# Optimization experiments

Hardware: AMD Instinct MI355X
Metric: run time of the kernel (lower is better)

## Reference

```python
import jax, jax.numpy as jnp
import numpy as np

B_SZ, NP, NTOK, D, H, DH, D2 = 8192, 10, 21, 128, 2, 64, 32
EPS = 1e-8
PATCH_POS = np.array([2 * k - 1 for k in range(1, NP + 1)])  # [1,3,...,19]
STAT_POS = np.array([0] + [2 * k for k in range(1, NP + 1)])  # [0,2,...,20]


def setup_inputs() -> dict:
    key = jax.random.key(0)
    ks = jax.random.split(key, 12)
    x = jax.random.normal(ks[0], (B_SZ, NTOK, D), jnp.float32)
    # rotary frequencies: unit-magnitude complex exp(i * pos * theta)
    inv_freq = 1.0 / (10000.0 ** (jnp.arange(D2, dtype=jnp.float32) / D2))
    ang = jnp.arange(NTOK, dtype=jnp.float32)[:, None] * inv_freq[None, :]  # [N, d2]
    fc_real, fc_imag = jnp.cos(ang), jnp.sin(ang)
    s = 1.0 / np.sqrt(D)
    g = 1.0 + 0.02 * jax.random.normal(ks[1], (D,), jnp.float32)
    Wqkv = s * jax.random.normal(ks[2], (D, 3 * D), jnp.float32)
    bqkv = jnp.zeros((3 * D,), jnp.float32)
    Wout = s * jax.random.normal(ks[3], (D, D), jnp.float32)
    bout = jnp.zeros((D,), jnp.float32)
    Wg = s * jax.random.normal(ks[4], (D, D), jnp.float32)
    bg = jnp.zeros((D,), jnp.float32)
    Wr = s * jax.random.normal(ks[5], (D, D), jnp.float32)
    br = jnp.zeros((D,), jnp.float32)
    # learned bias B: decoupled init 0.0, coupled patch<->stat pairs 2.0
    Bb = np.zeros((NTOK, NTOK), np.float32)
    Bb[PATCH_POS, STAT_POS[1:]] = 2.0
    Bb[STAT_POS[1:], PATCH_POS] = 2.0
    return dict(x=x, fc_real=fc_real, fc_imag=fc_imag, g=g, Wqkv=Wqkv, bqkv=bqkv,
                Wout=Wout, bout=bout, Wg=Wg, bg=bg, Wr=Wr, br=br, Bbias=jnp.asarray(Bb))


def _zcrmsnorm(x, g):
    x0 = x - x.mean(-1, keepdims=True)
    return x0 / jnp.sqrt(jnp.mean(x0 * x0, -1, keepdims=True) + EPS) * g


def _rope(t, fr, fi):
    # t: [B,H,N,DH] viewed as complex pairs [B,H,N,d2,2]; fr/fi: [N,d2]
    tr = t.reshape(*t.shape[:-1], D2, 2)
    a, b = tr[..., 0], tr[..., 1]
    out = jnp.stack([a * fr - b * fi, a * fi + b * fr], axis=-1)
    return out.reshape(t.shape)


def reference(x, fc_real, fc_imag, g, Wqkv, bqkv, Wout, bout, Wg, bg, Wr, br, Bbias):
    B, N, Dm = x.shape
    h = _zcrmsnorm(x, g)
    qkv = (h @ Wqkv + bqkv).reshape(B, N, 3, H, DH)
    q = qkv[:, :, 0].transpose(0, 2, 1, 3)  # [B,H,N,DH]
    k = qkv[:, :, 1].transpose(0, 2, 1, 3)
    v = qkv[:, :, 2].transpose(0, 2, 1, 3)
    fr, fi = fc_real[:N], fc_imag[:N]
    q, k = _rope(q, fr, fi), _rope(k, fr, fi)
    scale = 1.0 / np.sqrt(DH)
    scores = jnp.einsum('bhnd,bhmd->bhnm', q, k) * scale + Bbias[None, None]
    a_full = jax.nn.softmax(scores, axis=-1)
    y_full = jnp.einsum('bhnm,bhmd->bhnd', a_full, v)
    y_full = y_full.transpose(0, 2, 1, 3).reshape(B, N, Dm) @ Wout + bout
    # patch -> stat attention
    q_p, k_s, v_s = q[:, :, PATCH_POS], k[:, :, STAT_POS], v[:, :, STAT_POS]
    sc2 = jnp.einsum('bhnd,bhmd->bhnm', q_p, k_s) * scale
    a2 = jax.nn.softmax(sc2, axis=-1)
    y2 = jnp.einsum('bhnm,bhmd->bhnd', a2, v_s).transpose(0, 2, 1, 3).reshape(B, NP, Dm)
    y2 = y2 @ Wr + br
    h_patch = h[:, PATCH_POS]  # [B,NP,D]
    norms = jnp.linalg.norm(h_patch, axis=-1, keepdims=True)
    uncertainty = 1.0 - jax.nn.sigmoid(norms - norms.mean())
    gate = jax.nn.sigmoid(h_patch @ Wg + bg) * uncertainty
    y = y_full.at[:, PATCH_POS, :].add(gate * y2)
    return x + y
```

## Files before the change

### kernel.cpp

```cpp
#include <hip/hip_runtime.h>
#include <math.h>

#define NB   8192
#define NTOK 21
#define NP   10

typedef __bf16 bf16_t;
typedef __bf16 bf16x8 __attribute__((ext_vector_type(8)));
typedef __bf16 bf16x4 __attribute__((ext_vector_type(4)));
typedef float  f32x4  __attribute__((ext_vector_type(4)));

#define ROW128(r,c) ((r)*128 + ((c) ^ (((r)&7)<<3)))
#define VTIDX(d,m)  ((d)*32  + ((m) ^ (((d)&3)<<3)))
#define ATIDX(r,m)  ((r)*32  + ((m) ^ (((r)&3)<<3)))

#define MFMA(a,b,c) __builtin_amdgcn_mfma_f32_16x16x32_bf16((a),(b),(c),0,0,0)

__global__ __launch_bounds__(256) void k_wconv(
    const float* __restrict__ Wqkv, const float* __restrict__ Wout,
    const float* __restrict__ Wg,   const float* __restrict__ Wr,
    bf16_t* __restrict__ wq, bf16_t* __restrict__ wo,
    bf16_t* __restrict__ wgb, bf16_t* __restrict__ wrb)
{
    int i = blockIdx.x * 256 + threadIdx.x;
    if (i < 49152) {
        int k = i / 384, n = i - k * 384;
        wq[((k >> 3) * 384 + n) * 8 + (k & 7)] = (bf16_t)Wqkv[i];
    } else {
        int j = i - 49152;
        int sel = j >> 14;
        int t = j & 16383;
        int k = t >> 7, n = t & 127;
        const float* src = sel == 0 ? Wout : (sel == 1 ? Wg : Wr);
        bf16_t* dst = sel == 0 ? wo : (sel == 1 ? wgb : wrb);
        dst[((k >> 3) * 128 + n) * 8 + (k & 7)] = (bf16_t)src[t];
    }
}

__global__ __launch_bounds__(256) void k_norms(const float* __restrict__ x,
                                               const float* __restrict__ g,
                                               float* __restrict__ part)
{
    __shared__ float sd[4];
    const int wave = threadIdx.x >> 6, lane = threadIdx.x & 63;
    const int row = blockIdx.x * 4 + wave;
    const int b = row / NP, p = row - b * NP;
    const float* xr = x + (size_t)b * 2688 + (2 * p + 1) * 128;
    float a0 = xr[lane], a1 = xr[lane + 64];
    float s = a0 + a1, sq = a0 * a0 + a1 * a1;
    #pragma unroll
    for (int off = 32; off; off >>= 1) { s += __shfl_xor(s, off); sq += __shfl_xor(sq, off); }
    float mean = s * (1.0f / 128);
    float rstd = rsqrtf(sq * (1.0f / 128) - mean * mean + 1e-8f);
    float h0 = (a0 - mean) * rstd * g[lane];
    float h1 = (a1 - mean) * rstd * g[lane + 64];
    float n2 = h0 * h0 + h1 * h1;
    #pragma unroll
    for (int off = 32; off; off >>= 1) n2 += __shfl_xor(n2, off);
    if (lane == 0) sd[wave] = sqrtf(n2);
    __syncthreads();
    if (threadIdx.x == 0)
        atomicAdd(&part[(blockIdx.x & 63) * 16], sd[0] + sd[1] + sd[2] + sd[3]);
}

__global__ __launch_bounds__(256, 4) void k_main(
    const float* __restrict__ x,   const float* __restrict__ fcr,
    const float* __restrict__ fci, const float* __restrict__ g,
    const float* __restrict__ bqkv, const float* __restrict__ bout,
    const float* __restrict__ bg,   const float* __restrict__ br,
    const float* __restrict__ Bb,   const float* __restrict__ part,
    const bf16_t* __restrict__ wq,  const bf16_t* __restrict__ wo,
    const bf16_t* __restrict__ wgb, const bf16_t* __restrict__ wrb,
    float* __restrict__ out)
{
    __shared__ __align__(16) bf16_t hsb[32 * 128];
    __shared__ __align__(16) bf16_t reg1[32 * 128];
    __shared__ __align__(16) bf16_t reg2[32 * 128];
    __shared__ __align__(16) bf16_t reg3[128 * 32];
    __shared__ __align__(16) char  pool[5376];
    __shared__ float normv[11];

    float* fcs  = (float*)pool;
    float* fis  = (float*)pool + 672;
    float* att  = (float*)pool;
    float* att2 = (float*)(pool + 3696);
    bf16_t* y2bb = (bf16_t*)pool;

    const int tid = threadIdx.x;
    const int w = tid >> 6, l = tid & 63, l15 = l & 15, gq = l >> 4;
    const int b = blockIdx.x;
    const float* xb = x + (size_t)b * 2688;

    {
        const float4* c4 = (const float4*)fcr; float4* dc = (float4*)fcs;
        const float4* i4 = (const float4*)fci; float4* di = (float4*)fis;
        if (tid < 168) { dc[tid] = c4[tid]; di[tid] = i4[tid]; }
        for (int i = tid; i < 11 * 128; i += 256)
            hsb[(21 + (i >> 7)) * 128 + (i & 127)] = (bf16_t)0.f;
        if (tid < 64) {
            float s = part[tid * 16];
            #pragma unroll
            for (int off = 32; off; off >>= 1) s += __shfl_xor(s, off);
            if (tid == 0) normv[10] = s * (1.f / 81920.f);
        }
        for (int r = w; r < 21; r += 4) {
            float a0 = xb[r * 128 + l], a1 = xb[r * 128 + 64 + l];
            float s = a0 + a1, sq = a0 * a0 + a1 * a1;
            #pragma unroll
            for (int off = 32; off; off >>= 1) { s += __shfl_xor(s, off); sq += __shfl_xor(sq, off); }
            float mean = s * (1.0f / 128);
            float rstd = rsqrtf(sq * (1.0f / 128) - mean * mean + 1e-8f);
            float h0 = (a0 - mean) * rstd * g[l];
            float h1 = (a1 - mean) * rstd * g[l + 64];
            hsb[ROW128(r, l)]      = (bf16_t)h0;
            hsb[ROW128(r, l + 64)] = (bf16_t)h1;
            if (r & 1) {
                float n2 = h0 * h0 + h1 * h1;
                #pragma unroll
                for (int off = 32; off; off >>= 1) n2 += __shfl_xor(n2, off);
                if (l == 0) normv[r >> 1] = sqrtf(n2);
            }
        }
    }
    __syncthreads();

    {
        bf16x8 afr[2][4];
        #pragma unroll
        for (int mt = 0; mt < 2; mt++)
            #pragma unroll
            for (int ks = 0; ks < 4; ks++)
                afr[mt][ks] = *(const bf16x8*)&hsb[ROW128(mt * 16 + l15, ks * 32 + gq * 8)];
        #pragma unroll 2
        for (int q6 = 0; q6 < 6; ++q6) {
            int nt = w * 6 + q6;
            int n = nt * 16 + l15;
            bf16x8 bfr[4];
            #pragma unroll
            for (int ks = 0; ks < 4; ks++)
                bfr[ks] = *(const bf16x8*)&wq[((ks * 4 + gq) * 384 + n) * 8];
            float bias = bqkv[n];
            #pragma unroll
            for (int mt = 0; mt < 2; mt++) {
                f32x4 acc = {0.f, 0.f, 0.f, 0.f};
                #pragma unroll
                for (int ks = 0; ks < 4; ks++) acc = MFMA(afr[mt][ks], bfr[ks], acc);
                int rbase = mt * 16 + gq * 4;
                if (n < 256) {
                    int d = n & 63, j = d >> 1;
                    bool ev = !(d & 1);
                    bf16_t* dst = (n < 128) ? reg1 : reg2;
                    int cc = n & 127;
                    #pragma unroll
                    for (int i = 0; i < 4; i++) {
                        int r = rbase + i; int rr = r < 21 ? r : 0;
                        float v = acc[i] + bias;
                        float p = __shfl_xor(v, 1);
                        float fr = fcs[rr * 32 + j], fi = fis[rr * 32 + j];
                        float o = ev ? (v * fr - p * fi) : (p * fi + v * fr);
                        dst[ROW128(r, cc)] = (bf16_t)o;
                    }
                } else {
                    int d = n - 256;
                    bf16x4 pv;
                    #pragma unroll
                    for (int i = 0; i < 4; i++) pv[i] = (bf16_t)(acc[i] + bias);
                    *(bf16x4*)&reg3[VTIDX(d, rbase)] = pv;
                }
            }
        }
    }
    __syncthreads();

    {
        #pragma unroll
        for (int q2 = 0; q2 < 2; q2++) {
            int t = w * 2 + q2;
            int hh = t >> 2, mt = (t >> 1) & 1, nt = t & 1;
            f32x4 acc = {0.f, 0.f, 0.f, 0.f};
            #pragma unroll
            for (int ks = 0; ks < 2; ks++) {
                bf16x8 a  = *(const bf16x8*)&reg1[ROW128(mt * 16 + l15, hh * 64 + ks * 32 + gq * 8)];
                bf16x8 bb = *(const bf16x8*)&reg2[ROW128(nt * 16 + l15, hh * 64 + ks * 32 + gq * 8)];
                acc = MFMA(a, bb, acc);
            }
            int m = nt * 16 + l15;
            if (m < 21) {
                #pragma unroll
                for (int i = 0; i < 4; i++) {
                    int n = mt * 16 + gq * 4 + i;
                    if (n < 21) att[hh * 462 + n * 22 + m] = acc[i] * 0.125f + Bb[n * 21 + m];
                }
            }
        }
        if (w < 2) {
            int hh = w;
            int ra = 2 * l15 + 1; if (ra > 20) ra = 20;
            int rb = 2 * l15;     if (rb > 20) rb = 20;
            f32x4 acc = {0.f, 0.f, 0.f, 0.f};
            #pragma unroll
            for (int ks = 0; ks < 2; ks++) {
                bf16x8 a  = *(const bf16x8*)&reg1[ROW128(ra, hh * 64 + ks * 32 + gq * 8)];
                bf16x8 bb = *(const bf16x8*)&reg2[ROW128(rb, hh * 64 + ks * 32 + gq * 8)];
                acc = MFMA(a, bb, acc);
            }
            int s = l15;
            if (s < 11) {
                #pragma unroll
                for (int i = 0; i < 4; i++) {
                    int p = gq * 4 + i;
                    if (p < 10) att2[hh * 120 + p * 12 + s] = acc[i] * 0.125f;
                }
            }
        }
    }
    __syncthreads();

    if (tid < 42) {
        int hh = tid / 21, n = tid - hh * 21;
        float* row = &att[hh * 462 + n * 22];
        float mx = -1e30f;
        for (int m = 0; m < 21; m++) mx = fmaxf(mx, row[m]);
        float s = 0.f;
        for (int m = 0; m < 21; m++) { float e = __expf(row[m] - mx); row[m] = e; s += e; }
        float inv = 1.f / s;
        for (int m = 0; m < 21; m++) row[m] *= inv;
    } else if (tid >= 64 && tid < 84) {
        int t2 = tid - 64, hh = t2 / 10, p = t2 - hh * 10;
        float* row = &att2[hh * 120 + p * 12];
        float mx = -1e30f;
        for (int m = 0; m < 11; m++) mx = fmaxf(mx, row[m]);
        float s = 0.f;
        for (int m = 0; m < 11; m++) { float e = __expf(row[m] - mx); row[m] = e; s += e; }
        float inv = 1.f / s;
        for (int m = 0; m < 11; m++) row[m] *= inv;
    }
    __syncthreads();

    {
        bf16_t* attb  = reg1;
        bf16_t* att2e = reg1 + 2048;
        for (int i = tid; i < 2048; i += 256) {
            int hh = i >> 10, r = (i >> 5) & 31, m = i & 31;
            float v = (r < 21 && m < 21) ? att[hh * 462 + r * 22 + m] : 0.f;
            attb[hh * 1024 + ATIDX(r, m)] = (bf16_t)v;
        }
        for (int i = tid; i < 1024; i += 256) {
            int hh = i >> 9, p = (i >> 5) & 15, m = i & 31;
            float v = (p < 10 && m < 21 && !(m & 1)) ? att2[hh * 120 + p * 12 + (m >> 1)] : 0.f;
            att2e[hh * 512 + ATIDX(p, m)] = (bf16_t)v;
        }
    }
    __syncthreads();

    {
        bf16_t* attb  = reg1;
        bf16_t* att2e = reg1 + 2048;
        for (int t = w * 6; t < w * 6 + 6; ++t) {
            int hh, dloc, mt = 0, isY2;
            if (t < 16) { hh = t >> 3; mt = (t >> 2) & 1; dloc = hh * 64 + (t & 3) * 16 + l15; isY2 = 0; }
            else        { int u = t - 16; hh = u >> 2;    dloc = hh * 64 + (u & 3) * 16 + l15; isY2 = 1; }
            bf16x8 a;
            if (!isY2) { int r = mt * 16 + l15; a = *(const bf16x8*)&attb[hh * 1024 + ATIDX(r, gq * 8)]; }
            else       {                        a = *(const bf16x8*)&att2e[hh * 512 + ATIDX(l15, gq * 8)]; }
            bf16x8 bb = *(const bf16x8*)&reg3[VTIDX(dloc, gq * 8)];
            f32x4 acc = {0.f, 0.f, 0.f, 0.f};
            acc = MFMA(a, bb, acc);
            if (!isY2) {
                #pragma unroll
                for (int i = 0; i < 4; i++) reg2[ROW128(mt * 16 + gq * 4 + i, dloc)] = (bf16_t)acc[i];
            } else {
                #pragma unroll
                for (int i = 0; i < 4; i++) {
                    int rr2 = gq * 4 + i;
                    if (rr2 < 10) y2bb[ROW128(rr2, dloc)] = (bf16_t)acc[i];
                }
            }
        }
    }
    __syncthreads();

    {
        float mn = normv[10];
        float* gyb = (float*)reg3;
        #pragma unroll
        for (int q2 = 0; q2 < 2; q2++) {
            int nt = w * 2 + q2;
            int n = nt * 16 + l15;
            int yrow = l15 < 10 ? l15 : 0;
            f32x4 accg = {0.f, 0.f, 0.f, 0.f}, accr = {0.f, 0.f, 0.f, 0.f};
            #pragma unroll
            for (int ks = 0; ks < 4; ks++) {
                bf16x8 wgf = *(const bf16x8*)&wgb[((ks * 4 + gq) * 128 + n) * 8];
                bf16x8 wrf = *(const bf16x8*)&wrb[((ks * 4 + gq) * 128 + n) * 8];
                bf16x8 ha  = *(const bf16x8*)&hsb[ROW128(2 * l15 + 1, ks * 32 + gq * 8)];
                bf16x8 ya  = *(const bf16x8*)&y2bb[ROW128(yrow, ks * 32 + gq * 8)];
                accg = MFMA(ha, wgf, accg);
                accr = MFMA(ya, wrf, accr);
            }
            float bgc = bg[n], brc = br[n];
            #pragma unroll
            for (int i = 0; i < 4; i++) {
                int p = gq * 4 + i;
                if (p < 10) {
                    float gate = 1.f / (1.f + __expf(-(accg[i] + bgc)));
                    float u = 1.f - 1.f / (1.f + __expf(-(normv[p] - mn)));
                    gyb[p * 128 + n] = u * gate * (accr[i] + brc);
                }
            }
        }
    }
    __syncthreads();

    {
        float* gyb = (float*)reg3;
        float* ob = out + (size_t)b * 2688;
        for (int t = w * 4; t < w * 4 + 4; ++t) {
            int mt = t >> 3, nt = t & 7;
            int n = nt * 16 + l15;
            f32x4 acc = {0.f, 0.f, 0.f, 0.f};
            #pragma unroll
            for (int ks = 0; ks < 4; ks++) {
                bf16x8 a  = *(const bf16x8*)&reg2[ROW128(mt * 16 + l15, ks * 32 + gq * 8)];
                bf16x8 wf = *(const bf16x8*)&wo[((ks * 4 + gq) * 128 + n) * 8];
                acc = MFMA(a, wf, acc);
            }
            float bo = bout[n];
            #pragma unroll
            for (int i = 0; i < 4; i++) {
                int r = mt * 16 + gq * 4 + i;
                if (r < 21) {
                    float v = xb[r * 128 + n] + acc[i] + bo;
                    if (r & 1) v += gyb[((r - 1) >> 1) * 128 + n];
                    ob[r * 128 + n] = v;
                }
            }
        }
    }
}

extern "C" void kernel_launch(void* const* d_in, const int* in_sizes, int n_in,
                              void* d_out, int out_size, void* d_ws, size_t ws_size,
                              hipStream_t stream)
{
    (void)in_sizes; (void)n_in; (void)out_size; (void)ws_size;
    const float* x    = (const float*)d_in[0];
    const float* fcr  = (const float*)d_in[1];
    const float* fci  = (const float*)d_in[2];
    const float* g    = (const float*)d_in[3];
    const float* Wqkv = (const float*)d_in[4];
    const float* bqkv = (const float*)d_in[5];
    const float* Wout = (const float*)d_in[6];
    const float* bout = (const float*)d_in[7];
    const float* Wg   = (const float*)d_in[8];
    const float* bg   = (const float*)d_in[9];
    const float* Wr   = (const float*)d_in[10];
    const float* br   = (const float*)d_in[11];
    const float* Bb   = (const float*)d_in[12];
    float* out = (float*)d_out;

    char* wsb = (char*)d_ws;
    float* part = (float*)wsb;
    bf16_t* wq  = (bf16_t*)(wsb + 4096);
    bf16_t* wo  = wq + 49152;
    bf16_t* wgb = wo + 16384;
    bf16_t* wrb = wgb + 16384;

    hipMemsetAsync(part, 0, 4096, stream);
    hipLaunchKernelGGL(k_wconv, dim3(384),   dim3(256), 0, stream, Wqkv, Wout, Wg, Wr, wq, wo, wgb, wrb);
    hipLaunchKernelGGL(k_norms, dim3(20480), dim3(256), 0, stream, x, g, part);
    hipLaunchKernelGGL(k_main,  dim3(NB),    dim3(256), 0, stream,
                       x, fcr, fci, g, bqkv, bout, bg, br, Bb, part, wq, wo, wgb, wrb, out);
}
```

Before: 376.1 us.

## Fuse softmax into score MFMA epilogue and merge prep kernels

Merges the weight conversion and patch-norm kernels into one launch, with each norm block now handling 32 rows instead of 4. This cuts launch count and the number of atomics. In the main kernel, softmax for both attention paths now runs in registers with 16-lane shuffles right after the score MFMAs and writes bf16 probabilities straight into the swizzled MFMA operand layout. That removes the fp32 score buffer, a serial 42-thread softmax, a conversion pass and two barriers. In exchange it adds shuffles and uses more shared pool memory, which could affect occupancy.

```diff
diff --git a/kernel.cpp b/kernel.cpp
--- a/kernel.cpp
+++ b/kernel.cpp
@@ -16,51 +16,57 @@
 
 #define MFMA(a,b,c) __builtin_amdgcn_mfma_f32_16x16x32_bf16((a),(b),(c),0,0,0)
 
-__global__ __launch_bounds__(256) void k_wconv(
+__global__ __launch_bounds__(256) void k_prep(
     const float* __restrict__ Wqkv, const float* __restrict__ Wout,
     const float* __restrict__ Wg,   const float* __restrict__ Wr,
+    const float* __restrict__ x,    const float* __restrict__ g,
     bf16_t* __restrict__ wq, bf16_t* __restrict__ wo,
-    bf16_t* __restrict__ wgb, bf16_t* __restrict__ wrb)
-{
-    int i = blockIdx.x * 256 + threadIdx.x;
-    if (i < 49152) {
-        int k = i / 384, n = i - k * 384;
-        wq[((k >> 3) * 384 + n) * 8 + (k & 7)] = (bf16_t)Wqkv[i];
-    } else {
-        int j = i - 49152;
-        int sel = j >> 14;
-        int t = j & 16383;
-        int k = t >> 7, n = t & 127;
-        const float* src = sel == 0 ? Wout : (sel == 1 ? Wg : Wr);
-        bf16_t* dst = sel == 0 ? wo : (sel == 1 ? wgb : wrb);
-        dst[((k >> 3) * 128 + n) * 8 + (k & 7)] = (bf16_t)src[t];
-    }
-}
-
-__global__ __launch_bounds__(256) void k_norms(const float* __restrict__ x,
-                                               const float* __restrict__ g,
-                                               float* __restrict__ part)
+    bf16_t* __restrict__ wgb, bf16_t* __restrict__ wrb,
+    float* __restrict__ part)
 {
     __shared__ float sd[4];
-    const int wave = threadIdx.x >> 6, lane = threadIdx.x & 63;
-    const int row = blockIdx.x * 4 + wave;
-    const int b = row / NP, p = row - b * NP;
-    const float* xr = x + (size_t)b * 2688 + (2 * p + 1) * 128;
-    float a0 = xr[lane], a1 = xr[lane + 64];
-    float s = a0 + a1, sq = a0 * a0 + a1 * a1;
-    #pragma unroll
-    for (int off = 32; off; off >>= 1) { s += __shfl_xor(s, off); sq += __shfl_xor(sq, off); }
-    float mean = s * (1.0f / 128);
-    float rstd = rsqrtf(sq * (1.0f / 128) - mean * mean + 1e-8f);
-    float h0 = (a0 - mean) * rstd * g[lane];
-    float h1 = (a1 - mean) * rstd * g[lane + 64];
-    float n2 = h0 * h0 + h1 * h1;
-    #pragma unroll
-    for (int off = 32; off; off >>= 1) n2 += __shfl_xor(n2, off);
-    if (lane == 0) sd[wave] = sqrtf(n2);
-    __syncthreads();
-    if (threadIdx.x == 0)
-        atomicAdd(&part[(blockIdx.x & 63) * 16], sd[0] + sd[1] + sd[2] + sd[3]);
+    if (blockIdx.x < 384) {
+        int i = blockIdx.x * 256 + threadIdx.x;
+        if (i < 49152) {
+            int k = i / 384, n = i - k * 384;
+            wq[((k >> 3) * 384 + n) * 8 + (k & 7)] = (bf16_t)Wqkv[i];
+        } else {
+            int j = i - 49152;
+            int sel = j >> 14;
+            int t = j & 16383;
+            int k = t >> 7, n = t & 127;
+            const float* src = sel == 0 ? Wout : (sel == 1 ? Wg : Wr);
+            bf16_t* dst = sel == 0 ? wo : (sel == 1 ? wgb : wrb);
+            dst[((k >> 3) * 128 + n) * 8 + (k & 7)] = (bf16_t)src[t];
+        }
+    } else {
+        const int nb = blockIdx.x - 384;
+        const int wave = threadIdx.x >> 6, lane = threadIdx.x & 63;
+        const float g0v = g[lane], g1v = g[lane + 64];
+        float acc = 0.f;
+        #pragma unroll
+        for (int rr = 0; rr < 8; rr++) {
+            int row = nb * 32 + wave * 8 + rr;
+            int b = row / NP, p = row - b * NP;
+            const float* xr = x + (size_t)b * 2688 + (2 * p + 1) * 128;
+            float a0 = xr[lane], a1 = xr[lane + 64];
+            float s = a0 + a1, sq = a0 * a0 + a1 * a1;
+            #pragma unroll
+            for (int off = 32; off; off >>= 1) { s += __shfl_xor(s, off); sq += __shfl_xor(sq, off); }
+            float mean = s * (1.0f / 128);
+            float rstd = rsqrtf(sq * (1.0f / 128) - mean * mean + 1e-8f);
+            float h0 = (a0 - mean) * rstd * g0v;
+            float h1 = (a1 - mean) * rstd * g1v;
+            float n2 = h0 * h0 + h1 * h1;
+            #pragma unroll
+            for (int off = 32; off; off >>= 1) n2 += __shfl_xor(n2, off);
+            if (lane == 0) acc += sqrtf(n2);
+        }
+        if (lane == 0) sd[wave] = acc;
+        __syncthreads();
+        if (threadIdx.x == 0)
+            atomicAdd(&part[(nb & 63) * 16], sd[0] + sd[1] + sd[2] + sd[3]);
+    }
 }
 
 __global__ __launch_bounds__(256, 4) void k_main(
@@ -77,14 +83,11 @@
     __shared__ __align__(16) bf16_t reg1[32 * 128];
     __shared__ __align__(16) bf16_t reg2[32 * 128];
     __shared__ __align__(16) bf16_t reg3[128 * 32];
-    __shared__ __align__(16) char  pool[5376];
+    __shared__ __align__(16) char  pool[6144];
     __shared__ float normv[11];
 
     float* fcs  = (float*)pool;
     float* fis  = (float*)pool + 672;
-    float* att  = (float*)pool;
-    float* att2 = (float*)(pool + 3696);
-    bf16_t* y2bb = (bf16_t*)pool;
 
     const int tid = threadIdx.x;
     const int w = tid >> 6, l = tid & 63, l15 = l & 15, gq = l >> 4;
@@ -173,28 +176,43 @@
     __syncthreads();
 
     {
-        #pragma unroll
-        for (int q2 = 0; q2 < 2; q2++) {
-            int t = w * 2 + q2;
-            int hh = t >> 2, mt = (t >> 1) & 1, nt = t & 1;
-            f32x4 acc = {0.f, 0.f, 0.f, 0.f};
+        bf16_t* attb  = (bf16_t*)pool;
+        bf16_t* att2e = (bf16_t*)pool + 2048;
+        {
+            const int hh = w >> 1, mt = w & 1;
+            f32x4 acc0 = {0.f, 0.f, 0.f, 0.f}, acc1 = {0.f, 0.f, 0.f, 0.f};
             #pragma unroll
             for (int ks = 0; ks < 2; ks++) {
                 bf16x8 a  = *(const bf16x8*)&reg1[ROW128(mt * 16 + l15, hh * 64 + ks * 32 + gq * 8)];
-                bf16x8 bb = *(const bf16x8*)&reg2[ROW128(nt * 16 + l15, hh * 64 + ks * 32 + gq * 8)];
-                acc = MFMA(a, bb, acc);
-            }
-            int m = nt * 16 + l15;
-            if (m < 21) {
-                #pragma unroll
-                for (int i = 0; i < 4; i++) {
-                    int n = mt * 16 + gq * 4 + i;
-                    if (n < 21) att[hh * 462 + n * 22 + m] = acc[i] * 0.125f + Bb[n * 21 + m];
-                }
-            }
-        }
-        if (w < 2) {
-            int hh = w;
+                bf16x8 b0 = *(const bf16x8*)&reg2[ROW128(l15,           hh * 64 + ks * 32 + gq * 8)];
+                bf16x8 b1 = *(const bf16x8*)&reg2[ROW128(16 + l15,      hh * 64 + ks * 32 + gq * 8)];
+                acc0 = MFMA(a, b0, acc0);
+                acc1 = MFMA(a, b1, acc1);
+            }
+            const int m0 = l15, m1 = 16 + l15;
+            const bool c1 = (m1 < 21);
+            #pragma unroll
+            for (int i = 0; i < 4; i++) {
+                int r = mt * 16 + gq * 4 + i;
+                int rr = r < 21 ? r : 0;
+                float v0 = acc0[i] * 0.125f + Bb[rr * 21 + m0];
+                float v1 = c1 ? acc1[i] * 0.125f + Bb[rr * 21 + m1] : -1e30f;
+                float mx = fmaxf(v0, v1);
+                #pragma unroll
+                for (int off = 8; off; off >>= 1) mx = fmaxf(mx, __shfl_xor(mx, off));
+                float e0 = __expf(v0 - mx);
+                float e1 = c1 ? __expf(v1 - mx) : 0.f;
+                float s = e0 + e1;
+                #pragma unroll
+                for (int off = 8; off; off >>= 1) s += __shfl_xor(s, off);
+                float is = 1.f / s;
+                bool rv = (r < 21);
+                attb[hh * 1024 + ATIDX(r, m0)] = (bf16_t)(rv ? e0 * is : 0.f);
+                attb[hh * 1024 + ATIDX(r, m1)] = (bf16_t)(rv ? e1 * is : 0.f);
+            }
+        }
+        if ((w & 1) == 0) {
+            const int hh = w >> 1;
             int ra = 2 * l15 + 1; if (ra > 20) ra = 20;
             int rb = 2 * l15;     if (rb > 20) rb = 20;
             f32x4 acc = {0.f, 0.f, 0.f, 0.f};
@@ -204,58 +222,30 @@
                 bf16x8 bb = *(const bf16x8*)&reg2[ROW128(rb, hh * 64 + ks * 32 + gq * 8)];
                 acc = MFMA(a, bb, acc);
             }
-            int s = l15;
-            if (s < 11) {
-                #pragma unroll
-                for (int i = 0; i < 4; i++) {
-                    int p = gq * 4 + i;
-                    if (p < 10) att2[hh * 120 + p * 12 + s] = acc[i] * 0.125f;
-                }
-            }
-        }
-    }
-    __syncthreads();
-
-    if (tid < 42) {
-        int hh = tid / 21, n = tid - hh * 21;
-        float* row = &att[hh * 462 + n * 22];
-        float mx = -1e30f;
-        for (int m = 0; m < 21; m++) mx = fmaxf(mx, row[m]);
-        float s = 0.f;
-        for (int m = 0; m < 21; m++) { float e = __expf(row[m] - mx); row[m] = e; s += e; }
-        float inv = 1.f / s;
-        for (int m = 0; m < 21; m++) row[m] *= inv;
-    } else if (tid >= 64 && tid < 84) {
-        int t2 = tid - 64, hh = t2 / 10, p = t2 - hh * 10;
-        float* row = &att2[hh * 120 + p * 12];
-        float mx = -1e30f;
-        for (int m = 0; m < 11; m++) mx = fmaxf(mx, row[m]);
-        float s = 0.f;
-        for (int m = 0; m < 11; m++) { float e = __expf(row[m] - mx); row[m] = e; s += e; }
-        float inv = 1.f / s;
-        for (int m = 0; m < 11; m++) row[m] *= inv;
-    }
-    __syncthreads();
-
-    {
-        bf16_t* attb  = reg1;
-        bf16_t* att2e = reg1 + 2048;
-        for (int i = tid; i < 2048; i += 256) {
-            int hh = i >> 10, r = (i >> 5) & 31, m = i & 31;
-            float v = (r < 21 && m < 21) ? att[hh * 462 + r * 22 + m] : 0.f;
-            attb[hh * 1024 + ATIDX(r, m)] = (bf16_t)v;
-        }
-        for (int i = tid; i < 1024; i += 256) {
-            int hh = i >> 9, p = (i >> 5) & 15, m = i & 31;
-            float v = (p < 10 && m < 21 && !(m & 1)) ? att2[hh * 120 + p * 12 + (m >> 1)] : 0.f;
-            att2e[hh * 512 + ATIDX(p, m)] = (bf16_t)v;
-        }
-    }
-    __syncthreads();
-
-    {
-        bf16_t* attb  = reg1;
-        bf16_t* att2e = reg1 + 2048;
+            const bool cv = (l15 < 11);
+            #pragma unroll
+            for (int i = 0; i < 4; i++) {
+                int p = gq * 4 + i;
+                float v = cv ? acc[i] * 0.125f : -1e30f;
+                float mx = v;
+                #pragma unroll
+                for (int off = 8; off; off >>= 1) mx = fmaxf(mx, __shfl_xor(mx, off));
+                float e = cv ? __expf(v - mx) : 0.f;
+                float s = e;
+                #pragma unroll
+                for (int off = 8; off; off >>= 1) s += __shfl_xor(s, off);
+                float is = 1.f / s;
+                att2e[hh * 512 + ATIDX(p, 2 * l15)]     = (bf16_t)((p < 10) ? e * is : 0.f);
+                att2e[hh * 512 + ATIDX(p, 2 * l15 + 1)] = (bf16_t)0.f;
+            }
+        }
+    }
+    __syncthreads();
+
+    {
+        bf16_t* attb  = (bf16_t*)pool;
+        bf16_t* att2e = (bf16_t*)pool + 2048;
+        bf16_t* y2bb  = reg1;
         for (int t = w * 6; t < w * 6 + 6; ++t) {
             int hh, dloc, mt = 0, isY2;
             if (t < 16) { hh = t >> 3; mt = (t >> 2) & 1; dloc = hh * 64 + (t & 3) * 16 + l15; isY2 = 0; }
@@ -281,6 +271,7 @@
     __syncthreads();
 
     {
+        bf16_t* y2bb = reg1;
         float mn = normv[10];
         float* gyb = (float*)reg3;
         #pragma unroll
@@ -367,8 +358,8 @@
     bf16_t* wrb = wgb + 16384;
 
     hipMemsetAsync(part, 0, 4096, stream);
-    hipLaunchKernelGGL(k_wconv, dim3(384),   dim3(256), 0, stream, Wqkv, Wout, Wg, Wr, wq, wo, wgb, wrb);
-    hipLaunchKernelGGL(k_norms, dim3(20480), dim3(256), 0, stream, x, g, part);
-    hipLaunchKernelGGL(k_main,  dim3(NB),    dim3(256), 0, stream,
+    hipLaunchKernelGGL(k_prep, dim3(2944), dim3(256), 0, stream,
+                       Wqkv, Wout, Wg, Wr, x, g, wq, wo, wgb, wrb, part);
+    hipLaunchKernelGGL(k_main, dim3(NB),   dim3(256), 0, stream,
                        x, fcr, fci, g, bqkv, bout, bg, br, Bb, part, wq, wo, wgb, wrb, out);
 }
```

New measurement: 369.1 us. Within noise of the previous version (-1.9%).
